# Kernel tuning notes

Measured on AMD Instinct MI355X. Metric: run time of the kernel, lower is better.

Reference implementation:

```python
import jax, jax.numpy as jnp
import numpy as np

NUM_GRAPHS = 4096


def setup_inputs() -> dict:
    key = jax.random.key(0)
    k1, k2, k3, k4, k5 = jax.random.split(key, 5)
    N, H = 500000, 256
    x = jax.random.normal(k1, (N, H), dtype=jnp.float32)
    batch = jnp.sort(jax.random.randint(k2, (N,), 0, NUM_GRAPHS, dtype=jnp.int64))
    # gate MLP: Linear(H, H//2) -> tanh -> Linear(H//2, 1)
    W1 = jax.random.normal(k3, (H, H // 2), dtype=jnp.float32) / np.sqrt(H)
    b1 = jnp.zeros((H // 2,), dtype=jnp.float32)
    W2 = jax.random.normal(k4, (H // 2, 1), dtype=jnp.float32) / np.sqrt(H // 2)
    b2 = jnp.zeros((1,), dtype=jnp.float32)
    return {"x": x, "batch": batch, "W1": W1, "b1": b1, "W2": W2, "b2": b2}


def reference(x, batch, W1, b1, W2, b2):
    # gate scores per node: (N,)
    h = jnp.tanh(x @ W1 + b1)
    scores = (h @ W2 + b2).squeeze(-1)
    # segment (per-graph) softmax over nodes
    seg_max = jax.ops.segment_max(scores, batch, num_segments=NUM_GRAPHS)
    # empty segments give -inf max; guard so gather stays finite
    seg_max = jnp.where(jnp.isfinite(seg_max), seg_max, 0.0)
    ex = jnp.exp(scores - seg_max[batch])
    seg_sum = jax.ops.segment_sum(ex, batch, num_segments=NUM_GRAPHS)
    weights = ex / seg_sum[batch]  # (N,)
    # weighted scatter-add pooling -> (B, H)
    pooled = jax.ops.segment_sum(weights[:, None] * x, batch, num_segments=NUM_GRAPHS)
    return pooled, weights
```

## Files before the change

kernel.cpp:

```cpp
#include <hip/hip_runtime.h>
#include <hip/hip_bf16.h>

#define NGRAPH 4096
#define PBLOCKS 512

typedef __attribute__((ext_vector_type(8))) short s16x8;
typedef __attribute__((ext_vector_type(4))) float f32x4;
typedef unsigned int u32;

__device__ inline short f2bf(float f) {
  unsigned u = __float_as_uint(f);
  unsigned r = u + 0x7fffu + ((u >> 16) & 1u);
  return (short)(r >> 16);
}

__device__ inline long long getb(const void* b, int i, int is64) {
  if (is64) return ((const long long*)b)[i];
  return (long long)((const int*)b)[i];
}

__device__ inline int lowb(const void* b, int n, long long v, int is64) {
  int lo = 0, hi = n;
  while (lo < hi) {
    int mid = (lo + hi) >> 1;
    if (getb(b, mid, is64) < v) lo = mid + 1; else hi = mid;
  }
  return lo;
}

__device__ inline int batch_is64(const void* batch, int N) {
  int probe = ((N & 1) == 0) ? (N - 1) : (N - 2);
  return (((const int*)batch)[probe] == 0) ? 1 : 0;
}

__global__ void setup(const float* __restrict__ W1, const void* __restrict__ batch,
                      s16x8* __restrict__ w1p, int* __restrict__ offs,
                      int4* __restrict__ meta, float* __restrict__ pooled,
                      float* __restrict__ segsum, int N, int ntiles,
                      int metaB, int zeroB)
{
  const int b = blockIdx.x, tid = threadIdx.x;
  if (b < 16) {
    int t = b * 256 + tid;
    int f = t >> 6, l = t & 63;
    int kt = f >> 3, ct = f & 7;
    int k0 = kt * 32 + ((l >> 4) * 8);
    int c  = ct * 16 + (l & 15);
    s16x8 v;
    #pragma unroll
    for (int e = 0; e < 8; ++e) v[e] = f2bf(W1[(k0 + e) * 128 + c]);
    w1p[f * 64 + l] = v;
  } else if (b < 33) {
    const int is64 = batch_is64(batch, N);
    int g = (b - 16) * 256 + tid;
    if (g <= NGRAPH) offs[g] = lowb(batch, N, (long long)g, is64);
  } else if (b < 33 + metaB) {
    const int is64 = batch_is64(batch, N);
    int t = (b - 33) * 256 + tid;
    if (t < ntiles) {
      int node = t * 32; if (node >= N) node = N - 1;
      int g = (int)getb(batch, node, is64);
      meta[t] = make_int4(g,
                          lowb(batch, N, (long long)(g + 1), is64),
                          lowb(batch, N, (long long)(g + 2), is64),
                          lowb(batch, N, (long long)(g + 3), is64));
    }
  } else {
    const int zb = b - 33 - metaB;
    float4* p = (float4*)pooled;
    const int tot4 = NGRAPH * 256 / 4;
    for (int i = zb * 256 + tid; i < tot4; i += zeroB * 256)
      p[i] = make_float4(0.f, 0.f, 0.f, 0.f);
    for (int i = zb * 256 + tid; i < NGRAPH; i += zeroB * 256)
      segsum[i] = 0.f;
  }
}

__device__ inline float fast_tanh(float v) {
  v = fminf(fmaxf(v, -15.f), 15.f);
  float e = __expf(2.f * v);
  return __fdividef(e - 1.f, e + 1.f);
}

__device__ inline void dma16(const float* src, char* ldsdst) {
  __builtin_amdgcn_global_load_lds(
      (const __attribute__((address_space(1))) u32*)src,
      (__attribute__((address_space(3))) u32*)ldsdst,
      16, 0, 0);
}

__global__ __launch_bounds__(256, 2)
void gate_pool(const float* __restrict__ x, const int4* __restrict__ meta,
               const int* __restrict__ offs,
               const float* __restrict__ b1, const float* __restrict__ W2,
               const float* __restrict__ b2p, const s16x8* __restrict__ w1p,
               float* __restrict__ pooled, float* __restrict__ expout,
               float* __restrict__ segsum, int N, int ntiles)
{
  __shared__ __align__(16) char buf[2][32 * 1024];
  __shared__ float sp[2][32];
  __shared__ float sw[32];

  const int tid = threadIdx.x;
  const int w = tid >> 6, l = tid & 63;
  const int colhalf = w & 1, wp = w >> 1;
  const int l15 = l & 15, lg = l >> 4;

  if (blockIdx.x >= ntiles) return;

  s16x8 bf[4][8];
  #pragma unroll
  for (int ctl = 0; ctl < 4; ++ctl)
    #pragma unroll
    for (int kt = 0; kt < 8; ++kt)
      bf[ctl][kt] = w1p[(kt * 8 + colhalf * 4 + ctl) * 64 + l];

  float b1v[4], w2v[4];
  #pragma unroll
  for (int ct = 0; ct < 4; ++ct) {
    int c = colhalf * 64 + ct * 16 + l15;
    b1v[ct] = b1[c];
    w2v[ct] = W2[c];
  }
  const float b2s = b2p[0];

  int ti = blockIdx.x;
  int4 M = meta[ti];

  {
    const int node0 = ti * 32;
    #pragma unroll
    for (int i = 0; i < 8; ++i) {
      const int r = i * 4 + w;
      int grow = node0 + r;
      if (grow >= N) grow = N - 1;
      dma16(x + (size_t)grow * 256 + ((l ^ (r & 7)) << 2), buf[0] + r * 1024);
    }
  }
  asm volatile("s_waitcnt vmcnt(0)" ::: "memory");
  __builtin_amdgcn_s_barrier();
  __builtin_amdgcn_sched_barrier(0);

  int par = 0;
  for (; ti < ntiles; ti += PBLOCKS) {
    const int tnext = ti + PBLOCKS;
    int4 Mnext = M;
    if (tnext < ntiles) {
      Mnext = meta[tnext];
      const int nn0 = tnext * 32;
      char* dst = buf[par ^ 1];
      #pragma unroll
      for (int i = 0; i < 8; ++i) {
        const int r = i * 4 + w;
        int grow = nn0 + r;
        if (grow >= N) grow = N - 1;
        dma16(x + (size_t)grow * 256 + ((l ^ (r & 7)) << 2), dst + r * 1024);
      }
    }
    __builtin_amdgcn_sched_barrier(0);

    const char* tile = buf[par];
    const int node0 = ti * 32;

    {
      const int r0 = wp * 16 + l15;
      const char* p0 = tile + r0 * 1024;
      const int s0 = (r0 & 7);
      f32x4 acc0 = {0.f,0.f,0.f,0.f}, acc1 = {0.f,0.f,0.f,0.f};
      f32x4 acc2 = {0.f,0.f,0.f,0.f}, acc3 = {0.f,0.f,0.f,0.f};
      #pragma unroll
      for (int kt = 0; kt < 8; ++kt) {
        const int cc = kt * 8 + lg * 2;
        float4 xa = *(const float4*)(p0 + (((cc    ) ^ s0) << 4));
        float4 xb = *(const float4*)(p0 + (((cc + 1) ^ s0) << 4));
        s16x8 a;
        a[0] = f2bf(xa.x); a[1] = f2bf(xa.y); a[2] = f2bf(xa.z); a[3] = f2bf(xa.w);
        a[4] = f2bf(xb.x); a[5] = f2bf(xb.y); a[6] = f2bf(xb.z); a[7] = f2bf(xb.w);
        acc0 = __builtin_amdgcn_mfma_f32_16x16x32_bf16(a, bf[0][kt], acc0, 0, 0, 0);
        acc1 = __builtin_amdgcn_mfma_f32_16x16x32_bf16(a, bf[1][kt], acc1, 0, 0, 0);
        acc2 = __builtin_amdgcn_mfma_f32_16x16x32_bf16(a, bf[2][kt], acc2, 0, 0, 0);
        acc3 = __builtin_amdgcn_mfma_f32_16x16x32_bf16(a, bf[3][kt], acc3, 0, 0, 0);
      }
      float part[4];
      #pragma unroll
      for (int r = 0; r < 4; ++r) {
        part[r] = colhalf ? 0.f : b2s;
        part[r] += fast_tanh(acc0[r] + b1v[0]) * w2v[0];
        part[r] += fast_tanh(acc1[r] + b1v[1]) * w2v[1];
        part[r] += fast_tanh(acc2[r] + b1v[2]) * w2v[2];
        part[r] += fast_tanh(acc3[r] + b1v[3]) * w2v[3];
      }
      #pragma unroll
      for (int m = 1; m <= 8; m <<= 1) {
        #pragma unroll
        for (int r = 0; r < 4; ++r) part[r] += __shfl_xor(part[r], m, 64);
      }
      if (l15 == 0) {
        #pragma unroll
        for (int r = 0; r < 4; ++r)
          sp[colhalf][wp * 16 + lg * 4 + r] = part[r];
      }
    }
    asm volatile("s_waitcnt lgkmcnt(0)" ::: "memory");
    __builtin_amdgcn_s_barrier();
    __builtin_amdgcn_sched_barrier(0);

    if (tid < 32) {
      int node = node0 + tid;
      float e = 0.f;
      if (node < N) {
        e = __expf(sp[0][tid] + sp[1][tid]);
        expout[node] = e;
      }
      sw[tid] = e;
    }
    asm volatile("s_waitcnt lgkmcnt(0)" ::: "memory");
    __builtin_amdgcn_s_barrier();
    __builtin_amdgcn_sched_barrier(0);

    {
      const int nmax = min(32, N - node0);
      int g = M.x;
      int nb = M.y;
      int crossing = 0;
      const int ccb = tid >> 2, cib = (tid & 3) << 2;
      int r = 0;
      while (r < nmax) {
        const int rend = min(nb - node0, nmax);
        float pacc = 0.f, wsum = 0.f;
        for (; r + 8 <= rend; r += 8) {
          float xv[8], wv[8];
          #pragma unroll
          for (int u = 0; u < 8; ++u) {
            const int rr = r + u;
            xv[u] = *(const float*)(tile + rr * 1024 + (((ccb ^ (rr & 7)) << 4) | cib));
            wv[u] = sw[rr];
          }
          #pragma unroll
          for (int u = 0; u < 8; ++u) {
            pacc += wv[u] * xv[u];
            wsum += wv[u];
          }
        }
        for (; r < rend; ++r) {
          float wv = sw[r];
          pacc += wv * *(const float*)(tile + r * 1024 + (((ccb ^ (r & 7)) << 4) | cib));
          wsum += wv;
        }
        if (wsum > 0.f) {
          atomicAdd(&pooled[(size_t)g * 256 + tid], pacc);
          if (tid == 0) atomicAdd(&segsum[g], wsum);
        }
        if (rend >= nmax) break;
        ++g; ++crossing;
        nb = (crossing == 1) ? M.z
           : (crossing == 2) ? M.w
           : offs[min(g + 1, NGRAPH)];
      }
    }

    asm volatile("s_waitcnt vmcnt(0)" ::: "memory");
    __builtin_amdgcn_s_barrier();
    __builtin_amdgcn_sched_barrier(0);
    M = Mnext;
    par ^= 1;
  }
}

__global__ void finalize(float* __restrict__ pooled, float* __restrict__ wts,
                         const float* __restrict__ segsum,
                         const void* __restrict__ batch, int N)
{
  int f = blockIdx.x * 256 + threadIdx.x;
  if (f < NGRAPH * 256) {
    int g = f >> 8;
    float s = segsum[g];
    pooled[f] = (s > 0.f) ? pooled[f] / s : 0.f;
  } else {
    int n = f - NGRAPH * 256;
    if (n < N) {
      const int is64 = batch_is64(batch, N);
      int g = (int)getb(batch, n, is64);
      wts[n] = wts[n] / segsum[g];
    }
  }
}

extern "C" void kernel_launch(void* const* d_in, const int* in_sizes, int n_in,
                              void* d_out, int out_size, void* d_ws, size_t ws_size,
                              hipStream_t stream) {
  const float* x     = (const float*)d_in[0];
  const void*  batch = d_in[1];
  const float* W1    = (const float*)d_in[2];
  const float* b1    = (const float*)d_in[3];
  const float* W2    = (const float*)d_in[4];
  const float* b2    = (const float*)d_in[5];
  const int N = in_sizes[0] / 256;
  const int ntiles = (N + 31) / 32;

  float* pooled = (float*)d_out;
  float* wout   = (float*)d_out + (size_t)NGRAPH * 256;
  s16x8* w1p    = (s16x8*)d_ws;
  int*   offs   = (int*)((char*)d_ws + 64 * 1024);
  float* segsum = (float*)((char*)d_ws + 96 * 1024);
  int4*  meta   = (int4*)((char*)d_ws + 128 * 1024);

  const int metaB = (ntiles + 255) / 256;
  const int zeroB = 64;
  const int setupB = 33 + metaB + zeroB;

  setup<<<setupB, 256, 0, stream>>>(W1, batch, w1p, offs, meta,
                                    pooled, segsum, N, ntiles, metaB, zeroB);
  gate_pool<<<PBLOCKS, 256, 0, stream>>>(x, meta, offs, b1, W2, b2, w1p,
                                         pooled, wout, segsum, N, ntiles);
  const int tot = NGRAPH * 256 + N;
  finalize<<<(tot + 255) / 256, 256, 0, stream>>>(pooled, wout, segsum, batch, N);
}
```

Before: 177.6 us.

## Halve node tile to 16 rows and split gate columns across all four waves

Shrinks each tile from 32 to 16 nodes, so the LDS double buffer halves, and raises the occupancy target to 3 blocks per CU with 768 persistent blocks. Each wave now computes 32 hidden columns for all 16 rows instead of 64 columns for 16 rows. W1 fragments are reloaded from global or L2 every tile rather than held in 32 registers, which cuts register pressure. The cost is more per-tile overhead: twice as many barriers, meta entries and atomics per node, plus repeated weight loads.

Result: slower. 190.9 us (+7.5%).

```diff
diff --git a/kernel.cpp b/kernel.cpp
--- a/kernel.cpp
+++ b/kernel.cpp
@@ -2,7 +2,7 @@
 #include <hip/hip_bf16.h>
 
 #define NGRAPH 4096
-#define PBLOCKS 512
+#define PBLOCKS 768
 
 typedef __attribute__((ext_vector_type(8))) short s16x8;
 typedef __attribute__((ext_vector_type(4))) float f32x4;
@@ -58,7 +58,7 @@
     const int is64 = batch_is64(batch, N);
     int t = (b - 33) * 256 + tid;
     if (t < ntiles) {
-      int node = t * 32; if (node >= N) node = N - 1;
+      int node = t * 16; if (node >= N) node = N - 1;
       int g = (int)getb(batch, node, is64);
       meta[t] = make_int4(g,
                           lowb(batch, N, (long long)(g + 1), is64),
@@ -89,7 +89,7 @@
       16, 0, 0);
 }
 
-__global__ __launch_bounds__(256, 2)
+__global__ __launch_bounds__(256, 3)
 void gate_pool(const float* __restrict__ x, const int4* __restrict__ meta,
                const int* __restrict__ offs,
                const float* __restrict__ b1, const float* __restrict__ W2,
@@ -97,28 +97,20 @@
                float* __restrict__ pooled, float* __restrict__ expout,
                float* __restrict__ segsum, int N, int ntiles)
 {
-  __shared__ __align__(16) char buf[2][32 * 1024];
-  __shared__ float sp[2][32];
-  __shared__ float sw[32];
+  __shared__ __align__(16) char buf[2][16 * 1024];
+  __shared__ float sp[4][16];
+  __shared__ float sw[16];
 
   const int tid = threadIdx.x;
   const int w = tid >> 6, l = tid & 63;
-  const int colhalf = w & 1, wp = w >> 1;
   const int l15 = l & 15, lg = l >> 4;
 
   if (blockIdx.x >= ntiles) return;
 
-  s16x8 bf[4][8];
+  float b1v[2], w2v[2];
   #pragma unroll
-  for (int ctl = 0; ctl < 4; ++ctl)
-    #pragma unroll
-    for (int kt = 0; kt < 8; ++kt)
-      bf[ctl][kt] = w1p[(kt * 8 + colhalf * 4 + ctl) * 64 + l];
-
-  float b1v[4], w2v[4];
-  #pragma unroll
-  for (int ct = 0; ct < 4; ++ct) {
-    int c = colhalf * 64 + ct * 16 + l15;
+  for (int ct = 0; ct < 2; ++ct) {
+    int c = w * 32 + ct * 16 + l15;
     b1v[ct] = b1[c];
     w2v[ct] = W2[c];
   }
@@ -128,9 +120,9 @@
   int4 M = meta[ti];
 
   {
-    const int node0 = ti * 32;
+    const int node0 = ti * 16;
     #pragma unroll
-    for (int i = 0; i < 8; ++i) {
+    for (int i = 0; i < 4; ++i) {
       const int r = i * 4 + w;
       int grow = node0 + r;
       if (grow >= N) grow = N - 1;
@@ -143,14 +135,24 @@
 
   int par = 0;
   for (; ti < ntiles; ti += PBLOCKS) {
+    const int node0 = ti * 16;
+
+    s16x8 wb[8][2];
+    #pragma unroll
+    for (int kt = 0; kt < 8; ++kt) {
+      wb[kt][0] = w1p[(kt * 8 + w * 2    ) * 64 + l];
+      wb[kt][1] = w1p[(kt * 8 + w * 2 + 1) * 64 + l];
+    }
+    __builtin_amdgcn_sched_barrier(0);
+
     const int tnext = ti + PBLOCKS;
     int4 Mnext = M;
     if (tnext < ntiles) {
       Mnext = meta[tnext];
-      const int nn0 = tnext * 32;
+      const int nn0 = tnext * 16;
       char* dst = buf[par ^ 1];
       #pragma unroll
-      for (int i = 0; i < 8; ++i) {
+      for (int i = 0; i < 4; ++i) {
         const int r = i * 4 + w;
         int grow = nn0 + r;
         if (grow >= N) grow = N - 1;
@@ -160,14 +162,12 @@
     __builtin_amdgcn_sched_barrier(0);
 
     const char* tile = buf[par];
-    const int node0 = ti * 32;
 
     {
-      const int r0 = wp * 16 + l15;
+      const int r0 = l15;
       const char* p0 = tile + r0 * 1024;
       const int s0 = (r0 & 7);
       f32x4 acc0 = {0.f,0.f,0.f,0.f}, acc1 = {0.f,0.f,0.f,0.f};
-      f32x4 acc2 = {0.f,0.f,0.f,0.f}, acc3 = {0.f,0.f,0.f,0.f};
       #pragma unroll
       for (int kt = 0; kt < 8; ++kt) {
         const int cc = kt * 8 + lg * 2;
@@ -176,19 +176,15 @@
         s16x8 a;
         a[0] = f2bf(xa.x); a[1] = f2bf(xa.y); a[2] = f2bf(xa.z); a[3] = f2bf(xa.w);
         a[4] = f2bf(xb.x); a[5] = f2bf(xb.y); a[6] = f2bf(xb.z); a[7] = f2bf(xb.w);
-        acc0 = __builtin_amdgcn_mfma_f32_16x16x32_bf16(a, bf[0][kt], acc0, 0, 0, 0);
-        acc1 = __builtin_amdgcn_mfma_f32_16x16x32_bf16(a, bf[1][kt], acc1, 0, 0, 0);
-        acc2 = __builtin_amdgcn_mfma_f32_16x16x32_bf16(a, bf[2][kt], acc2, 0, 0, 0);
-        acc3 = __builtin_amdgcn_mfma_f32_16x16x32_bf16(a, bf[3][kt], acc3, 0, 0, 0);
+        acc0 = __builtin_amdgcn_mfma_f32_16x16x32_bf16(a, wb[kt][0], acc0, 0, 0, 0);
+        acc1 = __builtin_amdgcn_mfma_f32_16x16x32_bf16(a, wb[kt][1], acc1, 0, 0, 0);
       }
       float part[4];
       #pragma unroll
       for (int r = 0; r < 4; ++r) {
-        part[r] = colhalf ? 0.f : b2s;
+        part[r] = (w == 0) ? b2s : 0.f;
         part[r] += fast_tanh(acc0[r] + b1v[0]) * w2v[0];
         part[r] += fast_tanh(acc1[r] + b1v[1]) * w2v[1];
-        part[r] += fast_tanh(acc2[r] + b1v[2]) * w2v[2];
-        part[r] += fast_tanh(acc3[r] + b1v[3]) * w2v[3];
       }
       #pragma unroll
       for (int m = 1; m <= 8; m <<= 1) {
@@ -198,18 +194,18 @@
       if (l15 == 0) {
         #pragma unroll
         for (int r = 0; r < 4; ++r)
-          sp[colhalf][wp * 16 + lg * 4 + r] = part[r];
+          sp[w][lg * 4 + r] = part[r];
       }
     }
     asm volatile("s_waitcnt lgkmcnt(0)" ::: "memory");
     __builtin_amdgcn_s_barrier();
     __builtin_amdgcn_sched_barrier(0);
 
-    if (tid < 32) {
+    if (tid < 16) {
       int node = node0 + tid;
       float e = 0.f;
       if (node < N) {
-        e = __expf(sp[0][tid] + sp[1][tid]);
+        e = __expf(sp[0][tid] + sp[1][tid] + sp[2][tid] + sp[3][tid]);
         expout[node] = e;
       }
       sw[tid] = e;
@@ -219,7 +215,7 @@
     __builtin_amdgcn_sched_barrier(0);
 
     {
-      const int nmax = min(32, N - node0);
+      const int nmax = min(16, N - node0);
       int g = M.x;
       int nb = M.y;
       int crossing = 0;
@@ -228,16 +224,16 @@
       while (r < nmax) {
         const int rend = min(nb - node0, nmax);
         float pacc = 0.f, wsum = 0.f;
-        for (; r + 8 <= rend; r += 8) {
-          float xv[8], wv[8];
+        for (; r + 4 <= rend; r += 4) {
+          float xv[4], wv[4];
           #pragma unroll
-          for (int u = 0; u < 8; ++u) {
+          for (int u = 0; u < 4; ++u) {
             const int rr = r + u;
             xv[u] = *(const float*)(tile + rr * 1024 + (((ccb ^ (rr & 7)) << 4) | cib));
             wv[u] = sw[rr];
           }
           #pragma unroll
-          for (int u = 0; u < 8; ++u) {
+          for (int u = 0; u < 4; ++u) {
             pacc += wv[u] * xv[u];
             wsum += wv[u];
           }
@@ -296,7 +292,7 @@
   const float* W2    = (const float*)d_in[4];
   const float* b2    = (const float*)d_in[5];
   const int N = in_sizes[0] / 256;
-  const int ntiles = (N + 31) / 32;
+  const int ntiles = (N + 15) / 16;
 
   float* pooled = (float*)d_out;
   float* wout   = (float*)d_out + (size_t)NGRAPH * 256;
```
